# Optimization experiments

Measured on AMD Instinct MI355X. Metric: run time of the kernel, lower is better.

The kernel has to match this reference:

```python
import jax, jax.numpy as jnp
import numpy as np

NUM_HEADS = 4
D_MODEL = 192
NEG_INF = -1000000000.0  # fp32 branch of the original mask fill


def setup_inputs() -> dict:
    key = jax.random.key(0)
    ks = jax.random.split(key, 9)
    b, s, d = 4, 2048, D_MODEL
    inp = {
        "query": jax.random.normal(ks[0], (b, s, d), dtype=jnp.float32),
        "key": jax.random.normal(ks[1], (b, s, d), dtype=jnp.float32),
        "value": jax.random.normal(ks[2], (b, s, d), dtype=jnp.float32),
        "attn_mask": jax.random.randint(ks[3], (b, s, s), 0, 2, dtype=jnp.int32),
        "bias": jax.random.normal(ks[4], (1, NUM_HEADS, s, s), dtype=jnp.float32) * 0.1,
        # nn.Linear(d, d, bias=False) weights, applied as x @ W.T
        "Wq": jax.random.normal(ks[5], (d, d), dtype=jnp.float32) / np.sqrt(d),
        "Wk": jax.random.normal(ks[6], (d, d), dtype=jnp.float32) / np.sqrt(d),
        "Wv": jax.random.normal(ks[7], (d, d), dtype=jnp.float32) / np.sqrt(d),
        "Wo": jax.random.normal(ks[8], (d, d), dtype=jnp.float32) / np.sqrt(d),
    }
    return inp


def reference(query, key, value, attn_mask, bias, Wq, Wk, Wv, Wo):
    b, s, d = query.shape
    h, dh = NUM_HEADS, d // NUM_HEADS
    # QKV projections (Linear, no bias): x @ W.T
    q = (query @ Wq.T).reshape(b, s, h, dh)   # [b,s,h,dh]
    k = (key @ Wk.T).reshape(b, s, h, dh)
    v = (value @ Wv.T).reshape(b, s, h, dh)
    # unscaled dot-product logits (original has no 1/sqrt(d) scaling)
    logits = jnp.einsum("bqhd,bkhd->bhqk", q, k)
    logits = logits + bias                       # bias added BEFORE mask fill
    mask4 = attn_mask[:, None, :, :]             # [b,1,q,k] -> broadcast over heads
    logits = jnp.where(mask4 == 0, NEG_INF, logits)
    weights = jax.nn.softmax(logits, axis=-1)    # [b,h,q,k]
    # dropout_rate=0.0 (eval-mode / identity dropout)
    out = jnp.einsum("bhqk,bkhd->bqhd", weights, v).reshape(b, s, d)
    out = out @ Wo.T
    return out, weights.mean(axis=1)             # ([b,s,d], [b,s,s])
```

## Files before the change

### kernel.cpp

```cpp
#include <hip/hip_runtime.h>

#define BB 4
#define SS 2048
#define HH 4
#define DD 192
#define QT 16
#define NT (SS / 2 / 64)
#define NEG_BIG (-1e9f)
#define MB_NEG 0xCE6Eu

typedef __attribute__((ext_vector_type(8))) short short8;
typedef __attribute__((ext_vector_type(4))) float f32x4;

__device__ inline ushort f2bf(float x) {
    union { float f; unsigned u; } v; v.f = x;
    unsigned r = (v.u + 0x7FFFu + ((v.u >> 16) & 1u)) >> 16;
    return (ushort)r;
}
__device__ inline float bf2f(ushort x) {
    union { unsigned u; float f; } v; v.u = ((unsigned)x) << 16;
    return v.f;
}
__device__ inline void wave_lds_fence() {
    __builtin_amdgcn_wave_barrier();
    __builtin_amdgcn_s_waitcnt(0xC07F);
    __builtin_amdgcn_wave_barrier();
}

__global__ __launch_bounds__(256) void wt_kernel(
    const float* __restrict__ Wq, const float* __restrict__ Wk,
    const float* __restrict__ Wv, const float* __restrict__ Wo,
    float* __restrict__ WTall)
{
    __shared__ float tile[32][33];
    const float* W = (blockIdx.z == 0) ? Wq : (blockIdx.z == 1) ? Wk
                   : (blockIdx.z == 2) ? Wv : Wo;
    float* WT = WTall + (size_t)blockIdx.z * DD * DD;
    const int c0 = blockIdx.x * 32, j0 = blockIdx.y * 32;
    const int tx = threadIdx.x & 31, ty = threadIdx.x >> 5;
#pragma unroll
    for (int k = 0; k < 4; ++k)
        tile[ty + 8 * k][tx] = W[(size_t)(j0 + ty + 8 * k) * DD + c0 + tx];
    __syncthreads();
#pragma unroll
    for (int k = 0; k < 4; ++k)
        WT[(size_t)(c0 + ty + 8 * k) * DD + j0 + tx] = tile[tx][ty + 8 * k];
}

__global__ __launch_bounds__(192) void qkv_proj_kernel(
    const float* __restrict__ Xq, const float* __restrict__ Xk,
    const float* __restrict__ Xv, const float* __restrict__ WTall,
    ushort* __restrict__ qpad, ushort* __restrict__ kpadT,
    ushort* __restrict__ vTf)
{
    const int mode = blockIdx.y;
    const float* __restrict__ X = (mode == 0) ? Xq : (mode == 1) ? Xk : Xv;
    const float* __restrict__ WT = WTall + (size_t)mode * DD * DD;

    __shared__ __align__(16) float xs[16][DD];
    const int row0 = blockIdx.x * 16;
    const int t = threadIdx.x;
    {
        const float4* src = (const float4*)(X + (size_t)row0 * DD);
        float4* dst = (float4*)&xs[0][0];
        for (int i = t; i < 16 * DD / 4; i += 192) dst[i] = src[i];
    }
    __syncthreads();

    const int jt = (t % 48) * 4;
    const int rowg = t / 48;

    float acc[4][4];
#pragma unroll
    for (int r = 0; r < 4; ++r)
#pragma unroll
        for (int j = 0; j < 4; ++j) acc[r][j] = 0.f;

#pragma unroll 2
    for (int k4 = 0; k4 < DD / 4; ++k4) {
        float4 w0 = *(const float4*)&WT[(size_t)(k4 * 4 + 0) * DD + jt];
        float4 w1 = *(const float4*)&WT[(size_t)(k4 * 4 + 1) * DD + jt];
        float4 w2 = *(const float4*)&WT[(size_t)(k4 * 4 + 2) * DD + jt];
        float4 w3 = *(const float4*)&WT[(size_t)(k4 * 4 + 3) * DD + jt];
#pragma unroll
        for (int r = 0; r < 4; ++r) {
            float4 xv = *(const float4*)&xs[rowg * 4 + r][k4 * 4];
            acc[r][0] = fmaf(xv.x, w0.x, acc[r][0]); acc[r][1] = fmaf(xv.x, w0.y, acc[r][1]);
            acc[r][2] = fmaf(xv.x, w0.z, acc[r][2]); acc[r][3] = fmaf(xv.x, w0.w, acc[r][3]);
            acc[r][0] = fmaf(xv.y, w1.x, acc[r][0]); acc[r][1] = fmaf(xv.y, w1.y, acc[r][1]);
            acc[r][2] = fmaf(xv.y, w1.z, acc[r][2]); acc[r][3] = fmaf(xv.y, w1.w, acc[r][3]);
            acc[r][0] = fmaf(xv.z, w2.x, acc[r][0]); acc[r][1] = fmaf(xv.z, w2.y, acc[r][1]);
            acc[r][2] = fmaf(xv.z, w2.z, acc[r][2]); acc[r][3] = fmaf(xv.z, w2.w, acc[r][3]);
            acc[r][0] = fmaf(xv.w, w3.x, acc[r][0]); acc[r][1] = fmaf(xv.w, w3.y, acc[r][1]);
            acc[r][2] = fmaf(xv.w, w3.z, acc[r][2]); acc[r][3] = fmaf(xv.w, w3.w, acc[r][3]);
        }
    }

    const int b = row0 >> 11, s_base = row0 & (SS - 1);

    if (mode == 0) {
        const int hd = jt / 48, f = jt % 48;
#pragma unroll
        for (int r = 0; r < 4; ++r) {
            ushort4 o;
            o.x = f2bf(acc[r][0]); o.y = f2bf(acc[r][1]);
            o.z = f2bf(acc[r][2]); o.w = f2bf(acc[r][3]);
            *(ushort4*)&qpad[((size_t)(row0 + rowg * 4 + r) * HH + hd) * 64 + f] = o;
        }
        const int4 z = make_int4(0, 0, 0, 0);
        for (int i = t; i < 128; i += 192) {
            const int row = i >> 3, hh = (i >> 1) & 3, half = i & 1;
            *(int4*)&qpad[((size_t)(row0 + row) * HH + hh) * 64 + 48 + half * 8] = z;
        }
    } else if (mode == 1) {
        const int hd = jt / 48, f0 = jt % 48;
        const int off_base = (f0 < 32)
            ? ((f0 >> 3) * 16) * 8 + (f0 & 7)
            : 512 + (((f0 - 32) >> 3) * 16) * 8 + (f0 & 7);
#pragma unroll
        for (int r = 0; r < 4; ++r) {
            const int s = s_base + rowg * 4 + r;
            ushort4 o;
            o.x = f2bf(acc[r][0]); o.y = f2bf(acc[r][1]);
            o.z = f2bf(acc[r][2]); o.w = f2bf(acc[r][3]);
            const size_t base = ((size_t)(b * HH + hd) * (SS / 16) + (s >> 4)) * 1024;
            *(ushort4*)&kpadT[base + off_base + (size_t)(s & 15) * 8] = o;
        }
        const int4 z = make_int4(0, 0, 0, 0);
        for (int i = t; i < 128; i += 192) {
            const int row = i >> 3, hh = (i >> 1) & 3, half = i & 1;
            const int s = s_base + row;
            const size_t base = ((size_t)(b * HH + hh) * (SS / 16) + (s >> 4)) * 1024;
            *(int4*)&kpadT[base + 512 + ((size_t)((2 + half) * 16 + (s & 15))) * 8] = z;
        }
    } else {
#pragma unroll
        for (int j = 0; j < 4; ++j) {
            const int col = jt + j, hd = col / 48, f = col % 48;
            const int nb = f >> 4, dfrac = f & 15;
#pragma unroll
            for (int p = 0; p < 2; ++p) {
                const int s = s_base + rowg * 4 + 2 * p;
                unsigned pk = (unsigned)f2bf(acc[2 * p][j]) |
                              ((unsigned)f2bf(acc[2 * p + 1][j]) << 16);
                const size_t base =
                    (((size_t)(b * HH + hd) * (SS / 64) + (s >> 6)) * 3 + nb) * 1024;
                const int off = ((s & 63) >> 5) * 512 +
                                (((s & 31) >> 3) * 16 + dfrac) * 8 + (s & 7);
                *(unsigned*)&vTf[base + off] = pk;
            }
        }
    }
}

__global__ __launch_bounds__(512, 4) void attn_kernel(
    const ushort* __restrict__ qpad, const ushort* __restrict__ kpadT,
    const ushort* __restrict__ vTf, const int* __restrict__ mask,
    const float* __restrict__ bias,
    ushort* __restrict__ wscr, float* __restrict__ linv_g,
    float* __restrict__ oattn)
{
    __shared__ __align__(16) ushort wb[2][8][QT][72];
    __shared__ float l_scr[8][QT];

    const int b  = blockIdx.x >> 7;
    const int q0 = (blockIdx.x & 127) * QT;
    const int t = threadIdx.x;
    const int w = t >> 6;
    const int h = w & 3;
    const int kh = w >> 2;
    const int lane = t & 63;
    const int n16 = lane & 15, quad = lane >> 4;
    const int kbase0 = kh * (SS / 2);

    const ushort* qbase =
        qpad + ((size_t)(b * SS + q0 + n16) * HH + h) * 64 + quad * 8;
    const short8 qa0 = *(const short8*)(qbase);
    const short8 qa1 = *(const short8*)(qbase + 32);

    const ushort* kT = kpadT +
        ((size_t)(b * HH + h) * (SS / 16) + (kbase0 >> 4)) * 1024 + (size_t)lane * 8;
    const ushort* vTb = vTf +
        ((size_t)(b * HH + h) * (SS / 64) + (kbase0 >> 6)) * 3 * 1024 + (size_t)lane * 8;

    const int srow = lane >> 4;
    const int skey = (lane & 15) * 4;
    const int* mrow0 = mask + (size_t)(b * SS + q0) * SS + kbase0 + skey;
    const float* brow0 = bias + (size_t)(h * SS + q0) * SS + kbase0 + skey;

    float l_[4] = {0.f, 0.f, 0.f, 0.f};
    f32x4 pv[3];
#pragma unroll
    for (int nb = 0; nb < 3; ++nb) pv[nb] = (f32x4){0.f, 0.f, 0.f, 0.f};

    int4  mzc[4];
    float4 bvc[4];
#pragma unroll
    for (int rr = 0; rr < 4; ++rr) {
        const int row = rr * 4 + srow;
        mzc[rr] = *(const int4*)(mrow0 + (size_t)row * SS);
        bvc[rr] = *(const float4*)(brow0 + (size_t)row * SS);
    }
#pragma unroll
    for (int rr = 0; rr < 4; ++rr) {
        const int row = rr * 4 + srow;
        ushort4 o;
        o.x = mzc[rr].x ? f2bf(bvc[rr].x) : (ushort)MB_NEG;
        o.y = mzc[rr].y ? f2bf(bvc[rr].y) : (ushort)MB_NEG;
        o.z = mzc[rr].z ? f2bf(bvc[rr].z) : (ushort)MB_NEG;
        o.w = mzc[rr].w ? f2bf(bvc[rr].w) : (ushort)MB_NEG;
        *(ushort4*)&wb[0][w][row][skey] = o;
    }
#pragma unroll
    for (int rr = 0; rr < 4; ++rr) {
        const int row = rr * 4 + srow;
        mzc[rr] = *(const int4*)(mrow0 + (size_t)row * SS + 64);
        bvc[rr] = *(const float4*)(brow0 + (size_t)row * SS + 64);
    }
    wave_lds_fence();

    int buf = 0;
    for (int kt = 0; kt < NT; ++kt) {
        const int kb = kt * 64;

#pragma unroll
        for (int g = 0; g < 4; ++g) {
            const ushort* kp = kT + (size_t)(kt * 4 + g) * 1024;
            short8 kf0 = *(const short8*)(kp);
            short8 kf1 = *(const short8*)(kp + 512);
            f32x4 d = {0.f, 0.f, 0.f, 0.f};
            d = __builtin_amdgcn_mfma_f32_16x16x32_bf16(qa0, kf0, d, 0, 0, 0);
            d = __builtin_amdgcn_mfma_f32_16x16x32_bf16(qa1, kf1, d, 0, 0, 0);
#pragma unroll
            for (int r = 0; r < 4; ++r) {
                float wgt = __expf(d[r] + bf2f(wb[buf][w][quad * 4 + r][g * 16 + n16]));
                l_[r] += wgt;
                wb[buf][w][quad * 4 + r][g * 16 + n16] = f2bf(wgt);
            }
        }

        wave_lds_fence();

        if (kt + 1 < NT) {
#pragma unroll
            for (int rr = 0; rr < 4; ++rr) {
                const int row = rr * 4 + srow;
                ushort4 o;
                o.x = mzc[rr].x ? f2bf(bvc[rr].x) : (ushort)MB_NEG;
                o.y = mzc[rr].y ? f2bf(bvc[rr].y) : (ushort)MB_NEG;
                o.z = mzc[rr].z ? f2bf(bvc[rr].z) : (ushort)MB_NEG;
                o.w = mzc[rr].w ? f2bf(bvc[rr].w) : (ushort)MB_NEG;
                *(ushort4*)&wb[buf ^ 1][w][row][skey] = o;
            }
        }
        if (kt + 2 < NT) {
#pragma unroll
            for (int rr = 0; rr < 4; ++rr) {
                const int row = rr * 4 + srow;
                mzc[rr] = *(const int4*)(mrow0 + (size_t)row * SS + kb + 128);
                bvc[rr] = *(const float4*)(brow0 + (size_t)row * SS + kb + 128);
            }
        }

        const short8 wa0 = *(const short8*)&wb[buf][w][n16][quad * 8];
        const short8 wa1 = *(const short8*)&wb[buf][w][n16][32 + quad * 8];
#pragma unroll
        for (int nb = 0; nb < 3; ++nb) {
            const ushort* vp = vTb + (size_t)(kt * 3 + nb) * 1024;
            short8 v0 = *(const short8*)(vp);
            short8 v1 = *(const short8*)(vp + 512);
            pv[nb] = __builtin_amdgcn_mfma_f32_16x16x32_bf16(wa0, v0, pv[nb], 0, 0, 0);
            pv[nb] = __builtin_amdgcn_mfma_f32_16x16x32_bf16(wa1, v1, pv[nb], 0, 0, 0);
        }

        {
            const int r4 = lane >> 4;
            const int k4 = (lane & 15) * 4;
#pragma unroll
            for (int it = 0; it < 4; ++it) {
                const int row = it * 4 + r4;
                ushort4 wv = *(const ushort4*)&wb[buf][w][row][k4];
                *(ushort4*)&wscr[((size_t)(b * SS + q0 + row) * HH + h) * SS +
                                 kbase0 + kb + k4] = wv;
            }
        }

        wave_lds_fence();
        buf ^= 1;
    }

#pragma unroll
    for (int r = 0; r < 4; ++r) {
        float ll = l_[r];
#pragma unroll
        for (int off = 1; off < 16; off <<= 1) ll += __shfl_xor(ll, off);
        l_[r] = ll;
    }
    if (n16 == 0) {
#pragma unroll
        for (int r = 0; r < 4; ++r) l_scr[w][quad * 4 + r] = l_[r];
    }

    __syncthreads();

    float* scr = (float*)&wb[0][0][0][0];
    if (kh == 1) {
#pragma unroll
        for (int nb = 0; nb < 3; ++nb)
            *(f32x4*)&scr[((size_t)(h * 64 + lane)) * 12 + nb * 4] = pv[nb];
    }
    __syncthreads();

    if (kh == 0) {
        float linv[4];
#pragma unroll
        for (int r = 0; r < 4; ++r)
            linv[r] = 1.0f / (l_scr[h][quad * 4 + r] + l_scr[h + 4][quad * 4 + r]);
        if (n16 == 0) {
#pragma unroll
            for (int r = 0; r < 4; ++r)
                linv_g[((size_t)b * HH + h) * SS + q0 + quad * 4 + r] = linv[r];
        }
#pragma unroll
        for (int nb = 0; nb < 3; ++nb) {
            f32x4 po = *(const f32x4*)&scr[((size_t)(h * 64 + lane)) * 12 + nb * 4];
#pragma unroll
            for (int r = 0; r < 4; ++r)
                oattn[((size_t)(b * SS + q0 + quad * 4 + r)) * DD +
                      h * 48 + nb * 16 + n16] = (pv[nb][r] + po[r]) * linv[r];
        }
    }
}

__global__ __launch_bounds__(256) void tail_kernel(
    const float* __restrict__ X,
    const float* __restrict__ WT,
    float* __restrict__ Y,
    const ushort* __restrict__ wscr, const float* __restrict__ linv_g,
    float* __restrict__ out1)
{
    __shared__ __align__(16) float xs[16][DD];
    const int t = threadIdx.x;

    if (blockIdx.x < 512) {
        const int row0 = blockIdx.x * 16;
        {
            const float4* src = (const float4*)(X + (size_t)row0 * DD);
            float4* dst = (float4*)&xs[0][0];
            for (int i = t; i < 16 * DD / 4; i += 256) dst[i] = src[i];
        }
        __syncthreads();
        if (t < 192) {
            const int jt = (t % 48) * 4;
            const int rowg = t / 48;

            float acc[4][4];
#pragma unroll
            for (int r = 0; r < 4; ++r)
#pragma unroll
                for (int j = 0; j < 4; ++j) acc[r][j] = 0.f;

#pragma unroll 2
            for (int k4 = 0; k4 < DD / 4; ++k4) {
                float4 w0 = *(const float4*)&WT[(size_t)(k4 * 4 + 0) * DD + jt];
                float4 w1 = *(const float4*)&WT[(size_t)(k4 * 4 + 1) * DD + jt];
                float4 w2 = *(const float4*)&WT[(size_t)(k4 * 4 + 2) * DD + jt];
                float4 w3 = *(const float4*)&WT[(size_t)(k4 * 4 + 3) * DD + jt];
#pragma unroll
                for (int r = 0; r < 4; ++r) {
                    float4 xv = *(const float4*)&xs[rowg * 4 + r][k4 * 4];
                    acc[r][0] = fmaf(xv.x, w0.x, acc[r][0]); acc[r][1] = fmaf(xv.x, w0.y, acc[r][1]);
                    acc[r][2] = fmaf(xv.x, w0.z, acc[r][2]); acc[r][3] = fmaf(xv.x, w0.w, acc[r][3]);
                    acc[r][0] = fmaf(xv.y, w1.x, acc[r][0]); acc[r][1] = fmaf(xv.y, w1.y, acc[r][1]);
                    acc[r][2] = fmaf(xv.y, w1.z, acc[r][2]); acc[r][3] = fmaf(xv.y, w1.w, acc[r][3]);
                    acc[r][0] = fmaf(xv.z, w2.x, acc[r][0]); acc[r][1] = fmaf(xv.z, w2.y, acc[r][1]);
                    acc[r][2] = fmaf(xv.z, w2.z, acc[r][2]); acc[r][3] = fmaf(xv.z, w2.w, acc[r][3]);
                    acc[r][0] = fmaf(xv.w, w3.x, acc[r][0]); acc[r][1] = fmaf(xv.w, w3.y, acc[r][1]);
                    acc[r][2] = fmaf(xv.w, w3.z, acc[r][2]); acc[r][3] = fmaf(xv.w, w3.w, acc[r][3]);
                }
            }

#pragma unroll
            for (int r = 0; r < 4; ++r)
                *(float4*)&Y[(size_t)(row0 + rowg * 4 + r) * DD + jt] =
                    make_float4(acc[r][0], acc[r][1], acc[r][2], acc[r][3]);
        }
    } else {
        const int bq = blockIdx.x - 512;
        const int b = bq >> 11;
        const int q = bq & (SS - 1);
        const ushort* base = wscr + (size_t)bq * (HH * SS) + t * 8;

        float li[HH];
#pragma unroll
        for (int hh = 0; hh < HH; ++hh)
            li[hh] = linv_g[((size_t)b * HH + hh) * SS + q] * 0.25f;

        float acc[8];
#pragma unroll
        for (int j = 0; j < 8; ++j) acc[j] = 0.f;

#pragma unroll
        for (int hh = 0; hh < HH; ++hh) {
            short8 wv = *(const short8*)(base + (size_t)hh * SS);
#pragma unroll
            for (int j = 0; j < 8; ++j)
                acc[j] = fmaf(bf2f((ushort)wv[j]), li[hh], acc[j]);
        }

        float* dst = out1 + (size_t)bq * SS + t * 8;
        *(float4*)dst = make_float4(acc[0], acc[1], acc[2], acc[3]);
        *(float4*)(dst + 4) = make_float4(acc[4], acc[5], acc[6], acc[7]);
    }
}

extern "C" void kernel_launch(void* const* d_in, const int* in_sizes, int n_in,
                              void* d_out, int out_size, void* d_ws, size_t ws_size,
                              hipStream_t stream)
{
    const float* query = (const float*)d_in[0];
    const float* key   = (const float*)d_in[1];
    const float* value = (const float*)d_in[2];
    const int*   amask = (const int*)d_in[3];
    const float* bias  = (const float*)d_in[4];
    const float* Wq    = (const float*)d_in[5];
    const float* Wk    = (const float*)d_in[6];
    const float* Wv    = (const float*)d_in[7];
    const float* Wo    = (const float*)d_in[8];

    const size_t n_rows = (size_t)BB * SS;
    float* out0 = (float*)d_out;
    float* out1 = out0 + n_rows * DD;

    ushort* qpad  = (ushort*)d_ws;
    ushort* kpadT = qpad + n_rows * HH * 64;
    ushort* vTf   = kpadT + n_rows * HH * 64;
    float*  oattn = (float*)(vTf + (size_t)BB * HH * 48 * SS);
    float*  WTall = oattn + n_rows * DD;
    float*  linvg = WTall + 4 * DD * DD;
    ushort* wscr  = (ushort*)(linvg + (size_t)BB * HH * SS);

    wt_kernel<<<dim3(6, 6, 4), 256, 0, stream>>>(Wq, Wk, Wv, Wo, WTall);

    qkv_proj_kernel<<<dim3(n_rows / 16, 3), 192, 0, stream>>>(
        query, key, value, WTall, qpad, kpadT, vTf);

    attn_kernel<<<dim3(BB * SS / QT), 512, 0, stream>>>(
        qpad, kpadT, vTf, amask, bias, wscr, linvg, oattn);

    tail_kernel<<<dim3(512 + BB * SS), 256, 0, stream>>>(
        oattn, WTall + 3 * DD * DD, out0, wscr, linvg, out1);
}
```

Measured before the change: 347.9 us.

## Deepen mask/bias staging to four LDS buffers and pair QK/PV tiles

```diff
diff --git a/kernel.cpp b/kernel.cpp
--- a/kernel.cpp
+++ b/kernel.cpp
@@ -160,7 +160,7 @@
     ushort* __restrict__ wscr, float* __restrict__ linv_g,
     float* __restrict__ oattn)
 {
-    __shared__ __align__(16) ushort wb[2][8][QT][72];
+    __shared__ __align__(16) ushort wb[4][8][QT][72];
     __shared__ float l_scr[8][QT];
 
     const int b  = blockIdx.x >> 7;
@@ -195,34 +195,30 @@
 
     int4  mzc[4];
     float4 bvc[4];
-#pragma unroll
-    for (int rr = 0; rr < 4; ++rr) {
-        const int row = rr * 4 + srow;
-        mzc[rr] = *(const int4*)(mrow0 + (size_t)row * SS);
-        bvc[rr] = *(const float4*)(brow0 + (size_t)row * SS);
-    }
-#pragma unroll
-    for (int rr = 0; rr < 4; ++rr) {
-        const int row = rr * 4 + srow;
-        ushort4 o;
-        o.x = mzc[rr].x ? f2bf(bvc[rr].x) : (ushort)MB_NEG;
-        o.y = mzc[rr].y ? f2bf(bvc[rr].y) : (ushort)MB_NEG;
-        o.z = mzc[rr].z ? f2bf(bvc[rr].z) : (ushort)MB_NEG;
-        o.w = mzc[rr].w ? f2bf(bvc[rr].w) : (ushort)MB_NEG;
-        *(ushort4*)&wb[0][w][row][skey] = o;
-    }
-#pragma unroll
-    for (int rr = 0; rr < 4; ++rr) {
-        const int row = rr * 4 + srow;
-        mzc[rr] = *(const int4*)(mrow0 + (size_t)row * SS + 64);
-        bvc[rr] = *(const float4*)(brow0 + (size_t)row * SS + 64);
-    }
-    wave_lds_fence();
-
-    int buf = 0;
-    for (int kt = 0; kt < NT; ++kt) {
-        const int kb = kt * 64;
-
+
+    auto load_tile = [&](int kt) {
+#pragma unroll
+        for (int rr = 0; rr < 4; ++rr) {
+            const int row = rr * 4 + srow;
+            mzc[rr] = *(const int4*)(mrow0 + (size_t)row * SS + kt * 64);
+            bvc[rr] = *(const float4*)(brow0 + (size_t)row * SS + kt * 64);
+        }
+    };
+    auto stage_tile = [&](int kt) {
+        const int b4 = kt & 3;
+#pragma unroll
+        for (int rr = 0; rr < 4; ++rr) {
+            const int row = rr * 4 + srow;
+            ushort4 o;
+            o.x = mzc[rr].x ? f2bf(bvc[rr].x) : (ushort)MB_NEG;
+            o.y = mzc[rr].y ? f2bf(bvc[rr].y) : (ushort)MB_NEG;
+            o.z = mzc[rr].z ? f2bf(bvc[rr].z) : (ushort)MB_NEG;
+            o.w = mzc[rr].w ? f2bf(bvc[rr].w) : (ushort)MB_NEG;
+            *(ushort4*)&wb[b4][w][row][skey] = o;
+        }
+    };
+    auto qk_exp = [&](int kt) {
+        const int a4 = kt & 3;
 #pragma unroll
         for (int g = 0; g < 4; ++g) {
             const ushort* kp = kT + (size_t)(kt * 4 + g) * 1024;
@@ -233,37 +229,16 @@
             d = __builtin_amdgcn_mfma_f32_16x16x32_bf16(qa1, kf1, d, 0, 0, 0);
 #pragma unroll
             for (int r = 0; r < 4; ++r) {
-                float wgt = __expf(d[r] + bf2f(wb[buf][w][quad * 4 + r][g * 16 + n16]));
+                float wgt = __expf(d[r] + bf2f(wb[a4][w][quad * 4 + r][g * 16 + n16]));
                 l_[r] += wgt;
-                wb[buf][w][quad * 4 + r][g * 16 + n16] = f2bf(wgt);
+                wb[a4][w][quad * 4 + r][g * 16 + n16] = f2bf(wgt);
             }
         }
-
-        wave_lds_fence();
-
-        if (kt + 1 < NT) {
-#pragma unroll
-            for (int rr = 0; rr < 4; ++rr) {
-                const int row = rr * 4 + srow;
-                ushort4 o;
-                o.x = mzc[rr].x ? f2bf(bvc[rr].x) : (ushort)MB_NEG;
-                o.y = mzc[rr].y ? f2bf(bvc[rr].y) : (ushort)MB_NEG;
-                o.z = mzc[rr].z ? f2bf(bvc[rr].z) : (ushort)MB_NEG;
-                o.w = mzc[rr].w ? f2bf(bvc[rr].w) : (ushort)MB_NEG;
-                *(ushort4*)&wb[buf ^ 1][w][row][skey] = o;
-            }
-        }
-        if (kt + 2 < NT) {
-#pragma unroll
-            for (int rr = 0; rr < 4; ++rr) {
-                const int row = rr * 4 + srow;
-                mzc[rr] = *(const int4*)(mrow0 + (size_t)row * SS + kb + 128);
-                bvc[rr] = *(const float4*)(brow0 + (size_t)row * SS + kb + 128);
-            }
-        }
-
-        const short8 wa0 = *(const short8*)&wb[buf][w][n16][quad * 8];
-        const short8 wa1 = *(const short8*)&wb[buf][w][n16][32 + quad * 8];
+    };
+    auto pv_stream = [&](int kt) {
+        const int a4 = kt & 3;
+        const short8 wa0 = *(const short8*)&wb[a4][w][n16][quad * 8];
+        const short8 wa1 = *(const short8*)&wb[a4][w][n16][32 + quad * 8];
 #pragma unroll
         for (int nb = 0; nb < 3; ++nb) {
             const ushort* vp = vTb + (size_t)(kt * 3 + nb) * 1024;
@@ -272,21 +247,33 @@
             pv[nb] = __builtin_amdgcn_mfma_f32_16x16x32_bf16(wa0, v0, pv[nb], 0, 0, 0);
             pv[nb] = __builtin_amdgcn_mfma_f32_16x16x32_bf16(wa1, v1, pv[nb], 0, 0, 0);
         }
-
-        {
-            const int r4 = lane >> 4;
-            const int k4 = (lane & 15) * 4;
-#pragma unroll
-            for (int it = 0; it < 4; ++it) {
-                const int row = it * 4 + r4;
-                ushort4 wv = *(const ushort4*)&wb[buf][w][row][k4];
-                *(ushort4*)&wscr[((size_t)(b * SS + q0 + row) * HH + h) * SS +
-                                 kbase0 + kb + k4] = wv;
-            }
-        }
-
+        const int r4 = lane >> 4;
+        const int k4 = (lane & 15) * 4;
+#pragma unroll
+        for (int it = 0; it < 4; ++it) {
+            const int row = it * 4 + r4;
+            ushort4 wv = *(const ushort4*)&wb[a4][w][row][k4];
+            *(ushort4*)&wscr[((size_t)(b * SS + q0 + row) * HH + h) * SS +
+                             kbase0 + kt * 64 + k4] = wv;
+        }
+    };
+
+    load_tile(0); stage_tile(0);
+    load_tile(1); stage_tile(1);
+    load_tile(2);
+    wave_lds_fence();
+
+    for (int i = 0; i < NT / 2; ++i) {
+        const int a = 2 * i, bk = 2 * i + 1;
+        qk_exp(a);
+        if (a + 2 < NT) stage_tile(a + 2);
+        if (a + 3 < NT) load_tile(a + 3);
+        qk_exp(bk);
+        if (bk + 2 < NT) stage_tile(bk + 2);
+        if (bk + 3 < NT) load_tile(bk + 3);
         wave_lds_fence();
-        buf ^= 1;
+        pv_stream(a);
+        pv_stream(bk);
     }
 
 #pragma unroll
```

Measured after the change: 380.5 us. 9.4% more time.
